# Kernel tuning notes

Hardware: AMD Instinct MI355X
Metric: run time of the kernel (lower is better)

The kernel has to match this reference:

```python
import jax, jax.numpy as jnp
import numpy as np

DIM, DEPTH, HEADS, DIM_HEAD, MLP = 1024, 4, 16, 64, 4096
INNER = HEADS * DIM_HEAD
B, N = 2, 1024


def _ln(x, g, b, eps=1e-5):
    mu = jnp.mean(x, axis=-1, keepdims=True)
    var = jnp.mean(jnp.square(x - mu), axis=-1, keepdims=True)
    return (x - mu) * jax.lax.rsqrt(var + eps) * g + b


def setup_inputs() -> dict:
    key = jax.random.key(0)
    ks = jax.random.split(key, 8)
    s = 0.02
    return {
        "x": jax.random.normal(ks[0], (B, N, DIM), jnp.float32),
        "mask": jax.random.randint(ks[1], (B, N, N), 0, 2, jnp.int32),
        "ln1_g": jnp.ones((DEPTH, DIM), jnp.float32),
        "ln1_b": jnp.zeros((DEPTH, DIM), jnp.float32),
        "qkv_w": jax.random.normal(ks[2], (DEPTH, DIM, 3 * INNER), jnp.float32) * s,
        "out_w": jax.random.normal(ks[3], (DEPTH, INNER, DIM), jnp.float32) * s,
        "out_b": jnp.zeros((DEPTH, DIM), jnp.float32),
        "ln2_g": jnp.ones((DEPTH, DIM), jnp.float32),
        "ln2_b": jnp.zeros((DEPTH, DIM), jnp.float32),
        "ff1_w": jax.random.normal(ks[4], (DEPTH, DIM, MLP), jnp.float32) * s,
        "ff1_b": jnp.zeros((DEPTH, MLP), jnp.float32),
        "ff2_w": jax.random.normal(ks[5], (DEPTH, MLP, DIM), jnp.float32) * s,
        "ff2_b": jnp.zeros((DEPTH, DIM), jnp.float32),
    }


def reference(x, mask, ln1_g, ln1_b, qkv_w, out_w, out_b, ln2_g, ln2_b,
              ff1_w, ff1_b, ff2_w, ff2_b):
    scale = DIM_HEAD ** -0.5
    masked = (mask == 0)[:, None, :, :]  # [B,1,N,N], True -> fill -1e9
    b, n, _ = x.shape
    for l in range(DEPTH):
        # --- prenorm attention ---
        h = _ln(x, ln1_g[l], ln1_b[l])
        qkv = h @ qkv_w[l]  # [B,N,3*INNER]
        q, k, v = jnp.split(qkv, 3, axis=-1)
        q = q.reshape(b, n, HEADS, DIM_HEAD).transpose(0, 2, 1, 3)
        k = k.reshape(b, n, HEADS, DIM_HEAD).transpose(0, 2, 1, 3)
        v = v.reshape(b, n, HEADS, DIM_HEAD).transpose(0, 2, 1, 3)
        dots = jnp.einsum('bhqd,bhkd->bhqk', q, k) * scale
        dots = jnp.where(masked, jnp.float32(-1e9), dots)
        attn = jax.nn.softmax(dots, axis=-1)
        o = jnp.einsum('bhqk,bhkd->bhqd', attn, v)
        o = o.transpose(0, 2, 1, 3).reshape(b, n, INNER)
        x = o @ out_w[l] + out_b[l] + x
        # --- prenorm feedforward ---
        h = _ln(x, ln2_g[l], ln2_b[l])
        h = jax.nn.gelu(h @ ff1_w[l] + ff1_b[l], approximate=False)
        x = h @ ff2_w[l] + ff2_b[l] + x
    return x
```

## Files before the change

### kernel.cpp

```cpp
#include <hip/hip_runtime.h>
#include <stdint.h>

#define DIMM 1024
#define NSEQ 1024
#define BB 2
#define HEADSN 16
#define MLPD 4096
#define DEPTHN 4
#define MROWS (BB*NSEQ)
#define VSTR 10240

typedef __bf16 bf16x8 __attribute__((ext_vector_type(8)));
typedef float f32x4 __attribute__((ext_vector_type(4)));

__device__ __forceinline__ float bf2f(unsigned short u) {
    union { uint32_t i; float f; } x; x.i = ((uint32_t)u) << 16; return x.f;
}
__device__ __forceinline__ unsigned short f2bf(float f) {
    union { uint32_t i; float f; } x; x.f = f;
    uint32_t r = x.i + 0x7fffu + ((x.i >> 16) & 1u);
    return (unsigned short)(r >> 16);
}
__device__ __forceinline__ float loadf(const void* p, size_t i, int f32) {
    return f32 ? ((const float*)p)[i] : bf2f(((const unsigned short*)p)[i]);
}
__device__ __forceinline__ uint32_t cvt_pk_bf16(float lo, float hi) {
    uint32_t r;
    asm("v_cvt_pk_bf16_f32 %0, %1, %2" : "=v"(r) : "v"(lo), "v"(hi));
    return r;
}

__device__ __forceinline__ void gl_lds16(const unsigned short* g, unsigned short* l) {
    __builtin_amdgcn_global_load_lds(
        (const __attribute__((address_space(1))) uint32_t*)g,
        (__attribute__((address_space(3))) uint32_t*)l,
        16, 0, 0);
}

__device__ __forceinline__ void wait_vm4() { asm volatile("s_waitcnt vmcnt(4)" ::: "memory"); }
__device__ __forceinline__ void wait_vm0() { asm volatile("s_waitcnt vmcnt(0)" ::: "memory"); }
__device__ __forceinline__ void barrier_sync() {
    asm volatile("" ::: "memory");
    __builtin_amdgcn_s_barrier();
    asm volatile("" ::: "memory");
}

__global__ __launch_bounds__(256) void sniff_kernel(const unsigned short* __restrict__ x,
                                                    int* __restrict__ flag) {
    __shared__ int cnt[256];
    int tid = threadIdx.x;
    int c = 0;
    for (int i = tid * 2; i < 65536; i += 512) {
        int e = (x[i] >> 7) & 0xFF;
        if (e >= 0x8A) c++;
    }
    cnt[tid] = c;
    __syncthreads();
    for (int s = 128; s > 0; s >>= 1) {
        if (tid < s) cnt[tid] += cnt[tid + s];
        __syncthreads();
    }
    if (tid == 0) flag[0] = (cnt[0] > 32) ? 1 : 0;
}

__global__ __launch_bounds__(256) void store_out(const float* __restrict__ xf, void* __restrict__ out,
                                                 const int* __restrict__ flag) {
    int f = flag[0];
    int i = blockIdx.x * 256 + threadIdx.x;
    float v = xf[i];
    if (f) ((float*)out)[i] = v;
    else   ((unsigned short*)out)[i] = f2bf(v);
}
__global__ __launch_bounds__(256) void conv_all(const void* s0, const void* s1, const void* s2,
                                                const void* s3, const void* s4, const void* s5,
                                                const void* s6, unsigned short* __restrict__ dst,
                                                const int* __restrict__ flag) {
    int f = flag[0];
    const void* src; int len, off;
    switch (blockIdx.y) {
        case 0: src = s0; len = 1024; off = 0;    break;
        case 1: src = s1; len = 1024; off = 1024; break;
        case 2: src = s2; len = 1024; off = 2048; break;
        case 3: src = s3; len = 1024; off = 3072; break;
        case 4: src = s4; len = 1024; off = 4096; break;
        case 5: src = s5; len = 1024; off = 5120; break;
        default: src = s6; len = 4096; off = 6144; break;
    }
    int i = blockIdx.x * 256 + threadIdx.x;
    if (i < DEPTHN * len) {
        int l = i / len, o = i - l * len;
        dst[l * VSTR + off + o] = f2bf(loadf(src, i, f));
    }
}

__global__ __launch_bounds__(256) void transpose_conv(const void* __restrict__ in, size_t srcOffE,
                                                      unsigned short* __restrict__ out,
                                                      int K, int N, const int* __restrict__ flag) {
    int f = flag[0];
    __shared__ unsigned short t[32][33];
    int n0 = blockIdx.x * 32, k0 = blockIdx.y * 32;
    int tx = threadIdx.x, ty = threadIdx.y;
#pragma unroll
    for (int i = 0; i < 4; i++) {
        int k = k0 + ty + i * 8;
        t[ty + i * 8][tx] = f2bf(loadf(in, srcOffE + (size_t)k * N + n0 + tx, f));
    }
    __syncthreads();
#pragma unroll
    for (int i = 0; i < 4; i++) {
        int n = n0 + ty + i * 8;
        out[(size_t)n * K + k0 + tx] = t[tx][ty + i * 8];
    }
}

__global__ __launch_bounds__(256) void transpose_attn(const void* __restrict__ qkvw,
                                                      const void* __restrict__ outw,
                                                      int layer, unsigned short* __restrict__ wT,
                                                      const int* __restrict__ flag) {
    int f = flag[0];
    __shared__ unsigned short t[32][33];
    int id = blockIdx.x;
    const void* src; int N; size_t soff; unsigned short* dst; int bx, by;
    if (id < 3072) {
        N = 3072; bx = id % 96; by = id / 96;
        src = qkvw; soff = (size_t)layer * 1024 * 3072; dst = wT;
    } else {
        id -= 3072; N = 1024; bx = id % 32; by = id / 32;
        src = outw; soff = (size_t)layer * 1024 * 1024; dst = wT + 3 * 1024 * 1024;
    }
    int n0 = bx * 32, k0 = by * 32;
    int tx = threadIdx.x, ty = threadIdx.y;
#pragma unroll
    for (int i = 0; i < 4; i++) {
        int k = k0 + ty + i * 8;
        t[ty + i * 8][tx] = f2bf(loadf(src, soff + (size_t)k * N + n0 + tx, f));
    }
    __syncthreads();
#pragma unroll
    for (int i = 0; i < 4; i++) {
        int n = n0 + ty + i * 8;
        dst[(size_t)n * 1024 + k0 + tx] = t[tx][ty + i * 8];
    }
}

__global__ __launch_bounds__(256) void transpose_all(const void* __restrict__ qkvw,
                                                     const void* __restrict__ outw,
                                                     const void* __restrict__ ff1w,
                                                     const void* __restrict__ ff2w,
                                                     unsigned short* __restrict__ wTall,
                                                     const int* __restrict__ flag) {
    int f = flag[0];
    __shared__ unsigned short t[64 * 70];
    int id = blockIdx.x;
    int l = blockIdx.y;
    unsigned short* base = wTall + (size_t)l * (12u * 1024 * 1024);
    const void* src; int K, N; size_t soff; unsigned short* dst;
    if (id < 768)       { src = qkvw; K = 1024; N = 3072; soff = (size_t)l * 1024 * 3072; dst = base; }
    else if (id < 1024) { id -= 768;  src = outw; K = 1024; N = 1024; soff = (size_t)l * 1024 * 1024; dst = base + 3 * 1024 * 1024; }
    else if (id < 2048) { id -= 1024; src = ff1w; K = 1024; N = 4096; soff = (size_t)l * 1024 * 4096; dst = base + 4 * 1024 * 1024; }
    else                { id -= 2048; src = ff2w; K = 4096; N = 1024; soff = (size_t)l * 4096 * 1024; dst = base + 8 * 1024 * 1024; }
    int nb = N >> 6;
    int by = id / nb, bx = id - by * nb;
    int n0 = bx * 64, k0 = by * 64;
    int tid = threadIdx.x;
    int tx = tid & 15, ty = tid >> 4;
#pragma unroll
    for (int i = 0; i < 4; i++) {
        int r = ty + i * 16;
        size_t s = soff + (size_t)(k0 + r) * N + n0 + tx * 4;
        uint32_t w0, w1;
        if (f) {
            float4 v = *(const float4*)((const float*)src + s);
            w0 = cvt_pk_bf16(v.x, v.y);
            w1 = cvt_pk_bf16(v.z, v.w);
        } else {
            uint2 v = *(const uint2*)((const unsigned short*)src + s);
            w0 = v.x; w1 = v.y;
        }
        *(uint32_t*)&t[r * 70 + tx * 4]     = w0;
        *(uint32_t*)&t[r * 70 + tx * 4 + 2] = w1;
    }
    __syncthreads();
#pragma unroll
    for (int i = 0; i < 4; i++) {
        int n = ty + i * 16;
        ushort4 o;
        o.x = t[(tx * 4 + 0) * 70 + n];
        o.y = t[(tx * 4 + 1) * 70 + n];
        o.z = t[(tx * 4 + 2) * 70 + n];
        o.w = t[(tx * 4 + 3) * 70 + n];
        *(ushort4*)&dst[(size_t)(n0 + n) * K + k0 + tx * 4] = o;
    }
}

__global__ __launch_bounds__(256) void vt_kernel(const unsigned short* __restrict__ qkv,
                                                 unsigned short* __restrict__ vt) {
    __shared__ unsigned short t[64 * 70];
    int b = blockIdx.z;
    int c0 = blockIdx.x * 64, k0 = blockIdx.y * 64;
    int tid = threadIdx.x;
    int tx = tid & 15, ty = tid >> 4;
#pragma unroll
    for (int i = 0; i < 4; i++) {
        int r = ty + i * 16;
        uint2 v = *(const uint2*)&qkv[(size_t)(b * 1024 + k0 + r) * 3072 + 2048 + c0 + tx * 4];
        *(uint32_t*)&t[r * 70 + tx * 4]     = v.x;
        *(uint32_t*)&t[r * 70 + tx * 4 + 2] = v.y;
    }
    __syncthreads();
#pragma unroll
    for (int i = 0; i < 4; i++) {
        int c = ty + i * 16;
        ushort4 o;
        o.x = t[(tx * 4 + 0) * 70 + c];
        o.y = t[(tx * 4 + 1) * 70 + c];
        o.z = t[(tx * 4 + 2) * 70 + c];
        o.w = t[(tx * 4 + 3) * 70 + c];
        *(ushort4*)&vt[(size_t)(b * 1024 + c0 + c) * 1024 + k0 + tx * 4] = o;
    }
}

__global__ __launch_bounds__(256) void mask_pack(const int* __restrict__ mask,
                                                 unsigned long long* __restrict__ bits) {
    int wid = (blockIdx.x * 256 + threadIdx.x) >> 6;
    int lane = threadIdx.x & 63;
#pragma unroll
    for (int i = 0; i < 16; i++) {
        int w = wid * 16 + i;
        int mv = mask[(size_t)w * 64 + lane];
        unsigned long long bl = __ballot(mv != 0);
        if (lane == 0) bits[w] = bl;
    }
}

__global__ __launch_bounds__(256) void ln_raw(const void* __restrict__ x, float* __restrict__ xf,
                                              const unsigned short* __restrict__ g,
                                              const unsigned short* __restrict__ bta,
                                              unsigned short* __restrict__ out,
                                              const int* __restrict__ flag) {
    int f = flag[0];
    int row = blockIdx.x, tid = threadIdx.x;
    size_t base = (size_t)row * DIMM;
    float v[4]; float s = 0.f, s2 = 0.f;
#pragma unroll
    for (int i = 0; i < 4; i++) {
        int c = tid + i * 256;
        v[i] = loadf(x, base + c, f);
        xf[base + c] = v[i];
        s += v[i]; s2 += v[i] * v[i];
    }
#pragma unroll
    for (int off = 32; off >= 1; off >>= 1) {
        s  += __shfl_down(s, off, 64);
        s2 += __shfl_down(s2, off, 64);
    }
    __shared__ float rs[4], rs2[4];
    int wv = tid >> 6;
    if ((tid & 63) == 0) { rs[wv] = s; rs2[wv] = s2; }
    __syncthreads();
    s  = rs[0] + rs[1] + rs[2] + rs[3];
    s2 = rs2[0] + rs2[1] + rs2[2] + rs2[3];
    float mu  = s * (1.f / DIMM);
    float var = s2 * (1.f / DIMM) - mu * mu;
    float rr  = rsqrtf(var + 1e-5f);
#pragma unroll
    for (int i = 0; i < 4; i++) {
        int c = tid + i * 256;
        float y = (v[i] - mu) * rr * bf2f(g[c]) + bf2f(bta[c]);
        out[base + c] = f2bf(y);
    }
}

__global__ __launch_bounds__(256) void ln_kernel(const float* __restrict__ x,
                                                 const unsigned short* __restrict__ g,
                                                 const unsigned short* __restrict__ bta,
                                                 unsigned short* __restrict__ out) {
    int row = blockIdx.x, tid = threadIdx.x;
    const float* xr = x + (size_t)row * DIMM;
    float v[4]; float s = 0.f, s2 = 0.f;
#pragma unroll
    for (int i = 0; i < 4; i++) { v[i] = xr[tid + i * 256]; s += v[i]; s2 += v[i] * v[i]; }
#pragma unroll
    for (int off = 32; off >= 1; off >>= 1) {
        s  += __shfl_down(s, off, 64);
        s2 += __shfl_down(s2, off, 64);
    }
    __shared__ float rs[4], rs2[4];
    int wv = tid >> 6;
    if ((tid & 63) == 0) { rs[wv] = s; rs2[wv] = s2; }
    __syncthreads();
    s  = rs[0] + rs[1] + rs[2] + rs[3];
    s2 = rs2[0] + rs2[1] + rs2[2] + rs2[3];
    float mu  = s * (1.f / DIMM);
    float var = s2 * (1.f / DIMM) - mu * mu;
    float rr  = rsqrtf(var + 1e-5f);
#pragma unroll
    for (int i = 0; i < 4; i++) {
        int c = tid + i * 256;
        float y = (v[i] - mu) * rr * bf2f(g[c]) + bf2f(bta[c]);
        out[(size_t)row * DIMM + c] = f2bf(y);
    }
}

template <int S, int HAS_LN>
__global__ __launch_bounds__(256) void reduce_ln(const float* __restrict__ slab,
                                                 const unsigned short* __restrict__ bias,
                                                 float* __restrict__ xf,
                                                 const unsigned short* __restrict__ g,
                                                 const unsigned short* __restrict__ bta,
                                                 unsigned short* __restrict__ out) {
    const size_t SL = (size_t)MROWS * DIMM;
    int row = blockIdx.x, tid = threadIdx.x;
    float v[4]; float s = 0.f, s2 = 0.f;
#pragma unroll
    for (int i = 0; i < 4; i++) {
        int c = tid + i * 256;
        size_t idx = (size_t)row * DIMM + c;
        float t = xf[idx] + bf2f(bias[c]);
#pragma unroll
        for (int z = 0; z < S; z++) t += slab[z * SL + idx];
        xf[idx] = t;
        v[i] = t; s += t; s2 += t * t;
    }
    if (HAS_LN) {
#pragma unroll
        for (int off = 32; off >= 1; off >>= 1) {
            s  += __shfl_down(s, off, 64);
            s2 += __shfl_down(s2, off, 64);
        }
        __shared__ float rs[4], rs2[4];
        int wv = tid >> 6;
        if ((tid & 63) == 0) { rs[wv] = s; rs2[wv] = s2; }
        __syncthreads();
        s  = rs[0] + rs[1] + rs[2] + rs[3];
        s2 = rs2[0] + rs2[1] + rs2[2] + rs2[3];
        float mu  = s * (1.f / DIMM);
        float var = s2 * (1.f / DIMM) - mu * mu;
        float rr  = rsqrtf(var + 1e-5f);
#pragma unroll
        for (int i = 0; i < 4; i++) {
            int c = tid + i * 256;
            float y = (v[i] - mu) * rr * bf2f(g[c]) + bf2f(bta[c]);
            out[(size_t)row * DIMM + c] = f2bf(y);
        }
    }
}

template <int MODE, int SPLITK>
__global__ __launch_bounds__(512) void gemm_bt(const unsigned short* __restrict__ A,
                                               const unsigned short* __restrict__ Bt,
                                               const unsigned short* __restrict__ bias,
                                               unsigned short* __restrict__ Cbf,
                                               float* __restrict__ Cres,
                                               int M, int N, int K) {
    __shared__ __align__(16) unsigned short As0[128 * 64];
    __shared__ __align__(16) unsigned short Bs0[128 * 64];
    __shared__ __align__(16) unsigned short As1[128 * 64];
    __shared__ __align__(16) unsigned short Bs1[128 * 64];
    const int tid = threadIdx.x;
    const int mBase = blockIdx.y * 128, nBase = blockIdx.x * 128;
    const int w = tid >> 6, lane = tid & 63;
    const int wm = (w >> 2) * 64, wn = (w & 3) * 32;
    const int quad = lane >> 4, l16 = lane & 15;
    const int kLen = K / SPLITK;
    const int kStart = (SPLITK > 1) ? blockIdx.z * kLen : 0;
    const int NT = kLen / 64;

    f32x4 acc[4][2];
#pragma unroll
    for (int i = 0; i < 4; i++)
#pragma unroll
        for (int j = 0; j < 2; j++) acc[i][j] = (f32x4){0.f, 0.f, 0.f, 0.f};

    const int wb = w & 3;
    const int lr8 = lane >> 3;
    const int sgran = (lane & 7) ^ lr8;
    const unsigned short* G = (w < 4 ? A  + (size_t)(mBase + wb * 32 + lr8) * K
                                     : Bt + (size_t)(nBase + wb * 32 + lr8) * K)
                              + kStart + sgran * 8;
    unsigned short* S0 = (w < 4 ? As0 : Bs0) + (wb * 32) * 64;
    unsigned short* S1 = (w < 4 ? As1 : Bs1) + (wb * 32) * 64;
    const size_t r8 = (size_t)8 * K;

    const int rg0 = (quad ^ (l16 & 7)) * 8;
    const int rg1 = ((4 + quad) ^ (l16 & 7)) * 8;

    auto stage = [&](unsigned short* S, int t) {
        const unsigned short* g = G + (size_t)t * 64;
#pragma unroll
        for (int i = 0; i < 4; i++)
            gl_lds16(g + (size_t)i * r8, S + i * 8 * 64);
    };
    auto compute = [&](const unsigned short* Asb, const unsigned short* Bsb) {
#pragma unroll
        for (int ks = 0; ks < 2; ks++) {
            const int rg = ks ? rg1 : rg0;
            bf16x8 af[4], bfv[2];
#pragma unroll
            for (int i = 0; i < 4; i++)
                af[i] = *(const bf16x8*)&Asb[(wm + i * 16 + l16) * 64 + rg];
#pragma unroll
            for (int j = 0; j < 2; j++)
                bfv[j] = *(const bf16x8*)&Bsb[(wn + j * 16 + l16) * 64 + rg];
#pragma unroll
            for (int i = 0; i < 4; i++)
#pragma unroll
                for (int j = 0; j < 2; j++)
                    acc[i][j] = __builtin_amdgcn_mfma_f32_16x16x32_bf16(af[i], bfv[j], acc[i][j], 0, 0, 0);
        }
    };

    stage(S0, 0);
    for (int t = 0; t < NT; t += 2) {
        stage(S1, t + 1);
        wait_vm4();
        barrier_sync();
        compute(As0, Bs0);
        barrier_sync();
        if (t + 2 < NT) {
            stage(S0, t + 2);
            wait_vm4();
        } else {
            wait_vm0();
        }
        barrier_sync();
        compute(As1, Bs1);
        barrier_sync();
    }

    const size_t slabOff = (MODE == 3) ? (size_t)blockIdx.z * M * N : 0;
#pragma unroll
    for (int i = 0; i < 4; i++) {
#pragma unroll
        for (int j = 0; j < 2; j++) {
#pragma unroll
            for (int r = 0; r < 4; r++) {
                int m = mBase + wm + i * 16 + quad * 4 + r;
                int n = nBase + wn + j * 16 + l16;
                float v = acc[i][j][r];
                size_t idx = (size_t)m * N + n;
                if (MODE == 0) {
                    Cbf[idx] = f2bf(v);
                } else if (MODE == 1) {
                    if (SPLITK > 1) {
                        if (blockIdx.z == 0) v += bf2f(bias[n]);
                        atomicAdd(&Cres[idx], v);
                    } else {
                        Cres[idx] += v + bf2f(bias[n]);
                    }
                } else if (MODE == 2) {
                    float t2 = v + bf2f(bias[n]);
                    float gg = 0.5f * t2 * (1.f + erff(t2 * 0.70710678118f));
                    Cbf[idx] = f2bf(gg);
                } else {
                    Cres[slabOff + idx] = v;
                }
            }
        }
    }
}

__global__ __launch_bounds__(256) void attn_mfma(const unsigned short* __restrict__ qkv,
                                                 const unsigned short* __restrict__ vt,
                                                 const unsigned long long* __restrict__ mbits,
                                                 unsigned short* __restrict__ o) {
    __shared__ __align__(16) unsigned short Ks[2][64 * 72];
    __shared__ __align__(16) unsigned short Vs[2][64 * 72];

    const int tid = threadIdx.x, w = tid >> 6, lane = tid & 63;
    const int quad = lane >> 4, l16 = lane & 15;
    const int qt = blockIdx.x, h = blockIdx.y, b = blockIdx.z;

    const size_t qrow = (size_t)(b * NSEQ + qt * 64 + w * 16 + l16) * 3072 + h * 64;
    bf16x8 qf[2];
    qf[0] = *(const bf16x8*)(qkv + qrow + quad * 8);
    qf[1] = *(const bf16x8*)(qkv + qrow + 32 + quad * 8);

    const int srow = tid >> 2, scol = (tid & 3) * 16;
    const unsigned short* kg0 = qkv + (size_t)(b * NSEQ) * 3072 + 1024 + h * 64
                                + (size_t)srow * 3072 + scol;
    const unsigned short* vg0 = vt + (size_t)((b * HEADSN + h) * 64 + srow) * 1024 + scol;

    f32x4 oacc[4];
#pragma unroll
    for (int j = 0; j < 4; j++) oacc[j] = (f32x4){0.f, 0.f, 0.f, 0.f};
    float m_run = -1e30f, l_run = 0.f;

    const unsigned long long* mb = mbits + ((size_t)(b * NSEQ + qt * 64 + w * 16 + l16)) * 16;

    uint4 ka = *(const uint4*)kg0;
    uint4 kb = *(const uint4*)(kg0 + 8);
    uint4 va = *(const uint4*)vg0;
    uint4 vb = *(const uint4*)(vg0 + 8);
    *(uint4*)&Ks[0][srow * 72 + scol]     = ka;
    *(uint4*)&Ks[0][srow * 72 + scol + 8] = kb;
    *(uint4*)&Vs[0][srow * 72 + scol]     = va;
    *(uint4*)&Vs[0][srow * 72 + scol + 8] = vb;
    unsigned long long mw = mb[0];
    int cur = 0;

    for (int kt = 0; kt < 16; kt++) {
        __syncthreads();

        unsigned long long mw_n = 0;
        if (kt < 15) {
            const unsigned short* kg = kg0 + (size_t)(kt + 1) * 64 * 3072;
            ka = *(const uint4*)kg;
            kb = *(const uint4*)(kg + 8);
            const unsigned short* vg = vg0 + (kt + 1) * 64;
            va = *(const uint4*)vg;
            vb = *(const uint4*)(vg + 8);
            mw_n = mb[kt + 1];
        }

        f32x4 sacc[4];
#pragma unroll
        for (int j = 0; j < 4; j++) sacc[j] = (f32x4){0.f, 0.f, 0.f, 0.f};
        __builtin_amdgcn_s_setprio(1);
#pragma unroll
        for (int ks = 0; ks < 2; ks++) {
#pragma unroll
            for (int j = 0; j < 4; j++) {
                bf16x8 kf = *(const bf16x8*)&Ks[cur][(j * 16 + l16) * 72 + ks * 32 + quad * 8];
                sacc[j] = __builtin_amdgcn_mfma_f32_16x16x32_bf16(kf, qf[ks], sacc[j], 0, 0, 0);
            }
        }
        __builtin_amdgcn_s_setprio(0);

        float t[4][4];
        float mxj[4];
#pragma unroll
        for (int j = 0; j < 4; j++) {
            unsigned nib = (unsigned)(mw >> (quad * 4 + j * 16)) & 0xFu;
#pragma unroll
            for (int r = 0; r < 4; r++) {
                float s = sacc[j][r] * 0.125f;
                t[j][r] = ((nib >> r) & 1u) ? s : -1e30f;
            }
            mxj[j] = fmaxf(fmaxf(t[j][0], t[j][1]), fmaxf(t[j][2], t[j][3]));
        }
        float mx = fmaxf(fmaxf(mxj[0], mxj[1]), fmaxf(mxj[2], mxj[3]));
        mx = fmaxf(mx, __shfl_xor(mx, 16, 64));
        mx = fmaxf(mx, __shfl_xor(mx, 32, 64));

        if (!__all(mx <= m_run)) {
            float m_new = fmaxf(m_run, mx);
            float alpha = __expf(m_run - m_new);
            m_run = m_new;
            l_run *= alpha;
            float al[4];
#pragma unroll
            for (int r = 0; r < 4; r++) al[r] = __shfl(alpha, quad * 4 + r, 64);
#pragma unroll
            for (int j = 0; j < 4; j++)
#pragma unroll
                for (int r = 0; r < 4; r++) oacc[j][r] *= al[r];
        }

        float p[4][4];
        float psj[4];
#pragma unroll
        for (int j = 0; j < 4; j++) {
#pragma unroll
            for (int r = 0; r < 4; r++) p[j][r] = __expf(t[j][r] - m_run);
            psj[j] = (p[j][0] + p[j][1]) + (p[j][2] + p[j][3]);
        }
        float ps = (psj[0] + psj[1]) + (psj[2] + psj[3]);
        ps += __shfl_xor(ps, 16, 64);
        ps += __shfl_xor(ps, 32, 64);
        l_run += ps;

        union { uint32_t u[4]; bf16x8 v; } pa[2];
#pragma unroll
        for (int ks = 0; ks < 2; ks++) {
            pa[ks].u[0] = cvt_pk_bf16(p[2 * ks][0],     p[2 * ks][1]);
            pa[ks].u[1] = cvt_pk_bf16(p[2 * ks][2],     p[2 * ks][3]);
            pa[ks].u[2] = cvt_pk_bf16(p[2 * ks + 1][0], p[2 * ks + 1][1]);
            pa[ks].u[3] = cvt_pk_bf16(p[2 * ks + 1][2], p[2 * ks + 1][3]);
        }

        __builtin_amdgcn_s_setprio(1);
#pragma unroll
        for (int ks = 0; ks < 2; ks++) {
#pragma unroll
            for (int j = 0; j < 4; j++) {
                union { ushort4 u[2]; bf16x8 v; } vf;
                const unsigned short* vp = &Vs[cur][(j * 16 + l16) * 72 + ks * 32 + quad * 4];
                vf.u[0] = *(const ushort4*)vp;
                vf.u[1] = *(const ushort4*)(vp + 16);
                oacc[j] = __builtin_amdgcn_mfma_f32_16x16x32_bf16(pa[ks].v, vf.v, oacc[j], 0, 0, 0);
            }
        }
        __builtin_amdgcn_s_setprio(0);

        if (kt < 15) {
            *(uint4*)&Ks[cur ^ 1][srow * 72 + scol]     = ka;
            *(uint4*)&Ks[cur ^ 1][srow * 72 + scol + 8] = kb;
            *(uint4*)&Vs[cur ^ 1][srow * 72 + scol]     = va;
            *(uint4*)&Vs[cur ^ 1][srow * 72 + scol + 8] = vb;
            mw = mw_n;
            cur ^= 1;
        }
    }

    float inv[4];
#pragma unroll
    for (int r = 0; r < 4; r++) {
        float lr = __shfl(l_run, quad * 4 + r, 64);
        inv[r] = 1.f / lr;
    }
#pragma unroll
    for (int j = 0; j < 4; j++) {
#pragma unroll
        for (int r = 0; r < 4; r++) {
            size_t row = (size_t)(b * NSEQ + qt * 64 + w * 16 + quad * 4 + r);
            o[row * 1024 + h * 64 + j * 16 + l16] = f2bf(oacc[j][r] * inv[r]);
        }
    }
}

extern "C" void kernel_launch(void* const* d_in, const int* in_sizes, int n_in,
                              void* d_out, int out_size, void* d_ws, size_t ws_size,
                              hipStream_t stream) {
    const void* x     = d_in[0];
    const int*  mask  = (const int*)d_in[1];
    const void* ln1_g = d_in[2];
    const void* ln1_b = d_in[3];
    const void* qkv_w = d_in[4];
    const void* out_w = d_in[5];
    const void* out_b = d_in[6];
    const void* ln2_g = d_in[7];
    const void* ln2_b = d_in[8];
    const void* ff1_w = d_in[9];
    const void* ff1_b = d_in[10];
    const void* ff2_w = d_in[11];
    const void* ff2_b = d_in[12];

    char* ws = (char*)d_ws;
    float*          xf     = (float*)ws;
    unsigned short* h_bf   = (unsigned short*)(ws + (8u  << 20));
    unsigned short* qkv_bf = (unsigned short*)(ws + (12u << 20));
    unsigned short* ff_bf  = (unsigned short*)(ws + (12u << 20));
    unsigned short* vt_bf  = (unsigned short*)(ws + (24u << 20));
    unsigned short* o_bf   = (unsigned short*)(ws + (28u << 20));
    unsigned short* wT     = (unsigned short*)(ws + (32u << 20));
    unsigned short* vecs   = (unsigned short*)(ws + (40u << 20));
    int*            flag   = (int*)(ws + (40u << 20) + (128u << 10));
    unsigned long long* mbits = (unsigned long long*)(ws + (40u << 20) + (192u << 10));
    float*          slab   = (float*)(ws + (41u << 20));
    unsigned short* wTall  = (unsigned short*)(ws + (73ull << 20));

    const bool slabs_ok = ws_size >= (74ull << 20);
    const bool bigws    = ws_size >= (170ull << 20);

    sniff_kernel<<<1, 256, 0, stream>>>((const unsigned short*)x, flag);

    conv_all<<<dim3(64, 7), 256, 0, stream>>>(ln1_g, ln1_b, out_b, ln2_g, ln2_b, ff2_b, ff1_b,
                                              vecs, flag);
    mask_pack<<<512, 256, 0, stream>>>(mask, mbits);

    ln_raw<<<MROWS, 256, 0, stream>>>(x, xf, vecs + 0, vecs + 1024, h_bf, flag);

    if (bigws)
        transpose_all<<<dim3(3072, 4), 256, 0, stream>>>(
            qkv_w, out_w, ff1_w, ff2_w, wTall, flag);

    const int nx = MROWS * DIMM;

    for (int l = 0; l < DEPTHN; l++) {
        const unsigned short* lv = vecs + l * VSTR;
        const unsigned short* lvn = vecs + (l + 1) * VSTR;

        const unsigned short* lbase = bigws ? wTall + (size_t)l * (12u * 1024 * 1024) : wT;
        const unsigned short* qkvT = lbase;
        const unsigned short* outT = lbase + 3 * 1024 * 1024;
        const unsigned short* ff1T = bigws ? lbase + 4 * 1024 * 1024 : wT;
        const unsigned short* ff2T = bigws ? lbase + 8 * 1024 * 1024 : wT;

        if (!bigws)
            transpose_attn<<<4096, dim3(32, 8), 0, stream>>>(qkv_w, out_w, l, wT, flag);
        gemm_bt<0, 1><<<dim3(3072 / 128, MROWS / 128), 512, 0, stream>>>(
            h_bf, qkvT, nullptr, qkv_bf, nullptr, MROWS, 3072, 1024);
        vt_kernel<<<dim3(16, 16, BB), 256, 0, stream>>>(qkv_bf, vt_bf);
        attn_mfma<<<dim3(NSEQ / 64, HEADSN, BB), 256, 0, stream>>>(qkv_bf, vt_bf, mbits, o_bf);
        if (slabs_ok) {
            gemm_bt<3, 2><<<dim3(1024 / 128, MROWS / 128, 2), 512, 0, stream>>>(
                o_bf, outT, nullptr, nullptr, slab, MROWS, 1024, 1024);
            reduce_ln<2, 1><<<MROWS, 256, 0, stream>>>(
                slab, lv + 2048, xf, lv + 3072, lv + 4096, h_bf);
        } else {
            gemm_bt<1, 2><<<dim3(1024 / 128, MROWS / 128, 2), 512, 0, stream>>>(
                o_bf, outT, lv + 2048, nullptr, xf, MROWS, 1024, 1024);
            ln_kernel<<<MROWS, 256, 0, stream>>>(xf, lv + 3072, lv + 4096, h_bf);
        }

        if (!bigws)
            transpose_conv<<<dim3(4096 / 32, 1024 / 32), dim3(32, 8), 0, stream>>>(
                ff1_w, (size_t)l * 1024 * 4096, wT, 1024, 4096, flag);
        gemm_bt<2, 1><<<dim3(4096 / 128, MROWS / 128), 512, 0, stream>>>(
            h_bf, ff1T, lv + 6144, ff_bf, nullptr, MROWS, 4096, 1024);
        if (!bigws)
            transpose_conv<<<dim3(1024 / 32, 4096 / 32), dim3(32, 8), 0, stream>>>(
                ff2_w, (size_t)l * 4096 * 1024, wT, 4096, 1024, flag);
        if (slabs_ok) {
            gemm_bt<3, 4><<<dim3(1024 / 128, MROWS / 128, 4), 512, 0, stream>>>(
                ff_bf, ff2T, nullptr, nullptr, slab, MROWS, 1024, 4096);
            if (l < DEPTHN - 1)
                reduce_ln<4, 1><<<MROWS, 256, 0, stream>>>(
                    slab, lv + 5120, xf, lvn + 0, lvn + 1024, h_bf);
            else
                reduce_ln<4, 0><<<MROWS, 256, 0, stream>>>(
                    slab, lv + 5120, xf, nullptr, nullptr, nullptr);
        } else {
            gemm_bt<1, 4><<<dim3(1024 / 128, MROWS / 128, 4), 512, 0, stream>>>(
                ff_bf, ff2T, lv + 5120, nullptr, xf, MROWS, 1024, 4096);
            if (l < DEPTHN - 1)
                ln_kernel<<<MROWS, 256, 0, stream>>>(xf, lvn + 0, lvn + 1024, h_bf);
        }
    }

    store_out<<<nx / 256, 256, 0, stream>>>(xf, d_out, flag);
}
```

Before: 812.8 us.

## Fuse V transpose into QKV GEMM epilogue and widen weight-transpose stores

The QKV GEMM's V-column tiles now transpose their accumulators through LDS and write V^T directly, which removes the separate vt_kernel launch per layer. Those V tiles no longer write V into qkv_bf. The attention kernel reads only vt_bf for V, so this is consistent. The weight transpose kernel now writes 8-element vector stores instead of 4-element ones. The epilogue adds an extra LDS round trip and a barrier in the GEMM.

```diff
diff --git a/kernel.cpp b/kernel.cpp
--- a/kernel.cpp
+++ b/kernel.cpp
@@ -12,6 +12,7 @@
 
 typedef __bf16 bf16x8 __attribute__((ext_vector_type(8)));
 typedef float f32x4 __attribute__((ext_vector_type(4)));
+typedef unsigned short u16x8 __attribute__((ext_vector_type(8)));
 
 __device__ __forceinline__ float bf2f(unsigned short u) {
     union { uint32_t i; float f; } x; x.i = ((uint32_t)u) << 16; return x.f;
@@ -140,6 +141,33 @@
     for (int i = 0; i < 4; i++) {
         int n = n0 + ty + i * 8;
         dst[(size_t)n * 1024 + k0 + tx] = t[tx][ty + i * 8];
+    }
+}
+
+__global__ __launch_bounds__(256) void vt_kernel(const unsigned short* __restrict__ qkv,
+                                                 unsigned short* __restrict__ vt) {
+    __shared__ unsigned short t[64 * 70];
+    int b = blockIdx.z;
+    int c0 = blockIdx.x * 64, k0 = blockIdx.y * 64;
+    int tid = threadIdx.x;
+    int tx = tid & 15, ty = tid >> 4;
+#pragma unroll
+    for (int i = 0; i < 4; i++) {
+        int r = ty + i * 16;
+        uint2 v = *(const uint2*)&qkv[(size_t)(b * 1024 + k0 + r) * 3072 + 2048 + c0 + tx * 4];
+        *(uint32_t*)&t[r * 70 + tx * 4]     = v.x;
+        *(uint32_t*)&t[r * 70 + tx * 4 + 2] = v.y;
+    }
+    __syncthreads();
+#pragma unroll
+    for (int i = 0; i < 4; i++) {
+        int c = ty + i * 16;
+        ushort4 o;
+        o.x = t[(tx * 4 + 0) * 70 + c];
+        o.y = t[(tx * 4 + 1) * 70 + c];
+        o.z = t[(tx * 4 + 2) * 70 + c];
+        o.w = t[(tx * 4 + 3) * 70 + c];
+        *(ushort4*)&vt[(size_t)(b * 1024 + c0 + c) * 1024 + k0 + tx * 4] = o;
     }
 }
 
@@ -181,42 +209,14 @@
         *(uint32_t*)&t[r * 70 + tx * 4 + 2] = w1;
     }
     __syncthreads();
-#pragma unroll
-    for (int i = 0; i < 4; i++) {
-        int n = ty + i * 16;
-        ushort4 o;
-        o.x = t[(tx * 4 + 0) * 70 + n];
-        o.y = t[(tx * 4 + 1) * 70 + n];
-        o.z = t[(tx * 4 + 2) * 70 + n];
-        o.w = t[(tx * 4 + 3) * 70 + n];
-        *(ushort4*)&dst[(size_t)(n0 + n) * K + k0 + tx * 4] = o;
-    }
-}
-
-__global__ __launch_bounds__(256) void vt_kernel(const unsigned short* __restrict__ qkv,
-                                                 unsigned short* __restrict__ vt) {
-    __shared__ unsigned short t[64 * 70];
-    int b = blockIdx.z;
-    int c0 = blockIdx.x * 64, k0 = blockIdx.y * 64;
-    int tid = threadIdx.x;
-    int tx = tid & 15, ty = tid >> 4;
-#pragma unroll
-    for (int i = 0; i < 4; i++) {
-        int r = ty + i * 16;
-        uint2 v = *(const uint2*)&qkv[(size_t)(b * 1024 + k0 + r) * 3072 + 2048 + c0 + tx * 4];
-        *(uint32_t*)&t[r * 70 + tx * 4]     = v.x;
-        *(uint32_t*)&t[r * 70 + tx * 4 + 2] = v.y;
-    }
-    __syncthreads();
-#pragma unroll
-    for (int i = 0; i < 4; i++) {
-        int c = ty + i * 16;
-        ushort4 o;
-        o.x = t[(tx * 4 + 0) * 70 + c];
-        o.y = t[(tx * 4 + 1) * 70 + c];
-        o.z = t[(tx * 4 + 2) * 70 + c];
-        o.w = t[(tx * 4 + 3) * 70 + c];
-        *(ushort4*)&vt[(size_t)(b * 1024 + c0 + c) * 1024 + k0 + tx * 4] = o;
+    int tx2 = tid & 7, ty2 = tid >> 3;
+#pragma unroll
+    for (int i = 0; i < 2; i++) {
+        int n = ty2 + i * 32;
+        u16x8 o;
+#pragma unroll
+        for (int j = 0; j < 8; j++) o[j] = t[(tx2 * 8 + j) * 70 + n];
+        *(u16x8*)&dst[(size_t)(n0 + n) * K + k0 + tx2 * 8] = o;
     }
 }
 
@@ -352,11 +352,13 @@
                                                const unsigned short* __restrict__ bias,
                                                unsigned short* __restrict__ Cbf,
                                                float* __restrict__ Cres,
+                                               unsigned short* __restrict__ VtOut,
                                                int M, int N, int K) {
-    __shared__ __align__(16) unsigned short As0[128 * 64];
-    __shared__ __align__(16) unsigned short Bs0[128 * 64];
-    __shared__ __align__(16) unsigned short As1[128 * 64];
-    __shared__ __align__(16) unsigned short Bs1[128 * 64];
+    __shared__ __align__(16) unsigned short LDSbuf[4 * 128 * 64];
+    unsigned short* As0 = LDSbuf;
+    unsigned short* Bs0 = LDSbuf + 8192;
+    unsigned short* As1 = LDSbuf + 16384;
+    unsigned short* Bs1 = LDSbuf + 24576;
     const int tid = threadIdx.x;
     const int mBase = blockIdx.y * 128, nBase = blockIdx.x * 128;
     const int w = tid >> 6, lane = tid & 63;
@@ -426,6 +428,28 @@
         barrier_sync();
         compute(As1, Bs1);
         barrier_sync();
+    }
+
+    if (MODE == 0 && VtOut != nullptr && nBase >= 2048) {
+        unsigned short* T = LDSbuf;
+#pragma unroll
+        for (int i = 0; i < 4; i++)
+#pragma unroll
+            for (int j = 0; j < 2; j++)
+#pragma unroll
+                for (int r = 0; r < 4; r++)
+                    T[(wn + j * 16 + l16) * 136 + (wm + i * 16 + quad * 4 + r)] =
+                        f2bf(acc[i][j][r]);
+        barrier_sync();
+        const int b = mBase >> 10, kk = mBase & 1023;
+        const int tx = tid & 15, ty = tid >> 4;
+#pragma unroll
+        for (int p = 0; p < 4; p++) {
+            int c = ty + p * 32;
+            u16x8 val = *(const u16x8*)&T[c * 136 + tx * 8];
+            *(u16x8*)&VtOut[(size_t)(b * 1024 + (nBase - 2048) + c) * 1024 + kk + tx * 8] = val;
+        }
+        return;
     }
 
     const size_t slabOff = (MODE == 3) ? (size_t)blockIdx.z * M * N : 0;
@@ -680,17 +704,16 @@
         if (!bigws)
             transpose_attn<<<4096, dim3(32, 8), 0, stream>>>(qkv_w, out_w, l, wT, flag);
         gemm_bt<0, 1><<<dim3(3072 / 128, MROWS / 128), 512, 0, stream>>>(
-            h_bf, qkvT, nullptr, qkv_bf, nullptr, MROWS, 3072, 1024);
-        vt_kernel<<<dim3(16, 16, BB), 256, 0, stream>>>(qkv_bf, vt_bf);
+            h_bf, qkvT, nullptr, qkv_bf, nullptr, vt_bf, MROWS, 3072, 1024);
         attn_mfma<<<dim3(NSEQ / 64, HEADSN, BB), 256, 0, stream>>>(qkv_bf, vt_bf, mbits, o_bf);
         if (slabs_ok) {
             gemm_bt<3, 2><<<dim3(1024 / 128, MROWS / 128, 2), 512, 0, stream>>>(
-                o_bf, outT, nullptr, nullptr, slab, MROWS, 1024, 1024);
+                o_bf, outT, nullptr, nullptr, slab, nullptr, MROWS, 1024, 1024);
             reduce_ln<2, 1><<<MROWS, 256, 0, stream>>>(
                 slab, lv + 2048, xf, lv + 3072, lv + 4096, h_bf);
         } else {
             gemm_bt<1, 2><<<dim3(1024 / 128, MROWS / 128, 2), 512, 0, stream>>>(
-                o_bf, outT, lv + 2048, nullptr, xf, MROWS, 1024, 1024);
+                o_bf, outT, lv + 2048, nullptr, xf, nullptr, MROWS, 1024, 1024);
             ln_kernel<<<MROWS, 256, 0, stream>>>(xf, lv + 3072, lv + 4096, h_bf);
         }
 
@@ -698,13 +721,13 @@
             transpose_conv<<<dim3(4096 / 32, 1024 / 32), dim3(32, 8), 0, stream>>>(
                 ff1_w, (size_t)l * 1024 * 4096, wT, 1024, 4096, flag);
         gemm_bt<2, 1><<<dim3(4096 / 128, MROWS / 128), 512, 0, stream>>>(
-            h_bf, ff1T, lv + 6144, ff_bf, nullptr, MROWS, 4096, 1024);
+            h_bf, ff1T, lv + 6144, ff_bf, nullptr, nullptr, MROWS, 4096, 1024);
         if (!bigws)
             transpose_conv<<<dim3(1024 / 32, 4096 / 32), dim3(32, 8), 0, stream>>>(
                 ff2_w, (size_t)l * 4096 * 1024, wT, 4096, 1024, flag);
         if (slabs_ok) {
             gemm_bt<3, 4><<<dim3(1024 / 128, MROWS / 128, 4), 512, 0, stream>>>(
-                ff_bf, ff2T, nullptr, nullptr, slab, MROWS, 1024, 4096);
+                ff_bf, ff2T, nullptr, nullptr, slab, nullptr, MROWS, 1024, 4096);
             if (l < DEPTHN - 1)
                 reduce_ln<4, 1><<<MROWS, 256, 0, stream>>>(
                     slab, lv + 5120, xf, lvn + 0, lvn + 1024, h_bf);
@@ -713,7 +736,7 @@
                     slab, lv + 5120, xf, nullptr, nullptr, nullptr);
         } else {
             gemm_bt<1, 4><<<dim3(1024 / 128, MROWS / 128, 4), 512, 0, stream>>>(
-                ff_bf, ff2T, lv + 5120, nullptr, xf, MROWS, 1024, 4096);
+                ff_bf, ff2T, lv + 5120, nullptr, xf, nullptr, MROWS, 1024, 4096);
             if (l < DEPTHN - 1)
                 ln_kernel<<<MROWS, 256, 0, stream>>>(xf, lvn + 0, lvn + 1024, h_bf);
         }
```

New measurement: 812.7 us. Within noise of the previous version (-0.0%).
